# Kernel optimization log

Hardware: AMD Instinct MI355X
Metric: run time of the kernel (lower is better)

Reference implementation:

```python
import jax, jax.numpy as jnp
import numpy as np

N_NODES = 50000
N_EDGES = 800000


def gcn_conv(x, src, dst, W, b, n):
    # PyG GCNConv: add self-loops, symmetric normalization D^-1/2 (A+I) D^-1/2,
    # linear transform, scatter-add aggregation, then bias.
    loop = jnp.arange(n, dtype=src.dtype)
    src2 = jnp.concatenate([src, loop])
    dst2 = jnp.concatenate([dst, loop])
    deg = jax.ops.segment_sum(jnp.ones(src2.shape[0], x.dtype), dst2, num_segments=n)
    dis = jnp.where(deg > 0, jax.lax.rsqrt(jnp.maximum(deg, 1e-12)), 0.0)
    norm = dis[src2] * dis[dst2]                      # [E+N]
    xw = x @ W                                        # [N, out]
    msg = xw[src2] * norm[:, None]                    # [E+N, out] gather
    out = jax.ops.segment_sum(msg, dst2, num_segments=n)  # scatter-add
    return out + b


def setup_inputs() -> dict:
    key = jax.random.key(0)
    ks = jax.random.split(key, 8)
    d_in, d_h, d_out = 128, 128, 10
    x = jax.random.normal(ks[0], (N_NODES, d_in), dtype=jnp.float32)
    edge_index = jax.random.randint(ks[1], (2, N_EDGES), 0, N_NODES, dtype=jnp.int64)
    s = 1.0 / np.sqrt(d_in)
    W1 = jax.random.normal(ks[2], (d_in, d_h), dtype=jnp.float32) * s
    b1 = jnp.zeros((d_h,), jnp.float32)
    W2 = jax.random.normal(ks[3], (d_h, d_h), dtype=jnp.float32) * s
    b2 = jnp.zeros((d_h,), jnp.float32)
    W3 = jax.random.normal(ks[4], (d_h, d_out), dtype=jnp.float32) * s
    b3 = jnp.zeros((d_out,), jnp.float32)
    return {"x": x, "edge_index": edge_index, "W1": W1, "b1": b1,
            "W2": W2, "b2": b2, "W3": W3, "b3": b3}


def reference(x, edge_index, W1, b1, W2, b2, W3, b3):
    n = x.shape[0]
    src, dst = edge_index[0], edge_index[1]
    h = gcn_conv(x, src, dst, W1, b1, n)
    h = jax.nn.relu(h)
    # dropout(p=0.5) is identity in eval mode (training=False)
    h = gcn_conv(h, src, dst, W2, b2, n)
    h = gcn_conv(h, src, dst, W3, b3, n)
    return jax.nn.log_softmax(h, axis=1)
```

## Files before the change

### kernel.cpp

```cpp
#include <hip/hip_runtime.h>
#include <cstdint>
#include <cstddef>


typedef unsigned int uint;
typedef unsigned short u16;
typedef uint  uint4e  __attribute__((ext_vector_type(4)));
typedef float float4e __attribute__((ext_vector_type(4)));
typedef float float2e __attribute__((ext_vector_type(2)));
typedef uint  uint2e  __attribute__((ext_vector_type(2)));
typedef int   int2e   __attribute__((ext_vector_type(2)));
typedef int   int4e   __attribute__((ext_vector_type(4)));
using bf16x8 = __attribute__((ext_vector_type(8))) short;
using f32x4  = __attribute__((ext_vector_type(4))) float;

__device__ __forceinline__ float bf_lo(uint v) { return __uint_as_float(v << 16); }
__device__ __forceinline__ float bf_hi(uint v) { return __uint_as_float(v & 0xffff0000u); }
__device__ __forceinline__ u16 bf16_1(float a) {
    uint ua = __float_as_uint(a);
    ua = (ua + 0x7fffu + ((ua >> 16) & 1u)) >> 16;
    return (u16)ua;
}
__device__ __forceinline__ uint pack_bf2(float a, float b) {
    return (uint)bf16_1(a) | ((uint)bf16_1(b) << 16);
}

__global__ __launch_bounds__(256) void passA_wt(const int* __restrict__ ei, int E,
        int* __restrict__ cntA, int nbkt, int nca,
        const float* __restrict__ W1, const float* __restrict__ W2,
        const float* __restrict__ W3, const float* __restrict__ b2,
        u16* __restrict__ Wt1, float* __restrict__ W23, float* __restrict__ b23) {
    int tid = threadIdx.x, b = blockIdx.x;
    if (b < nca) {
        __shared__ int h[256];
        h[tid] = 0;
        __syncthreads();
        int ch = (E + nca - 1) / nca;
        int beg = b * ch, end = min(beg + ch, E);
        for (int e = beg + tid; e < end; e += 256)
            atomicAdd(&h[ei[E + e] >> 8], 1);
        __syncthreads();
        if (tid < nbkt) cntA[tid * nca + b] = h[tid];
    } else if (b == nca) {
        for (int i = 0; i < 64; ++i) {
            int idx = tid + i * 256;
            int k = idx >> 7, c = idx & 127;
            Wt1[c * 128 + k] = bf16_1(W1[idx]);
        }
        int c = tid >> 4, j0 = tid & 15;
        float acc = 0.f;
        if (c < 10) {
#pragma unroll
            for (int j = 0; j < 128; j += 16)
                acc += b2[j + j0] * W3[(j + j0) * 10 + c];
        }
#pragma unroll
        for (int m = 1; m < 16; m <<= 1) acc += __shfl_xor(acc, m);
        if (c < 10 && j0 == 0) b23[c] = acc;
    } else {
        __shared__ float w3s[1280];
        for (int i = tid; i < 1280; i += 256) w3s[i] = W3[i];
        __syncthreads();
        int idx = (b - nca - 1) * 256 + tid;
        int k = idx / 10, c = idx % 10;
        const float* w2r = W2 + (size_t)k * 128;
        float a0 = 0.f, a1 = 0.f, a2 = 0.f, a3 = 0.f;
#pragma unroll
        for (int j = 0; j < 128; j += 4) {
            a0 += w2r[j + 0] * w3s[(j + 0) * 10 + c];
            a1 += w2r[j + 1] * w3s[(j + 1) * 10 + c];
            a2 += w2r[j + 2] * w3s[(j + 2) * 10 + c];
            a3 += w2r[j + 3] * w3s[(j + 3) * 10 + c];
        }
        W23[idx] = (a0 + a1) + (a2 + a3);
    }
}

__global__ __launch_bounds__(256) void scan1(int* __restrict__ cntA, int nca,
        int* __restrict__ btot) {
    __shared__ int s[256];
    int b = blockIdx.x, tid = threadIdx.x;
    int v = cntA[b * nca + tid];
    s[tid] = v;
    __syncthreads();
    for (int d = 1; d < 256; d <<= 1) {
        int t = (tid >= d) ? s[tid - d] : 0;
        __syncthreads();
        s[tid] += t;
        __syncthreads();
    }
    cntA[b * nca + tid] = s[tid] - v;
    if (tid == 255) btot[b] = s[255];
}

__global__ __launch_bounds__(256) void passB(const int* __restrict__ ei, int E,
        const int* __restrict__ cntA, int nca, int nbkt,
        const int* __restrict__ btot, int2e* __restrict__ ebkt) {
    __shared__ int sc[256];
    __shared__ int cur[256];
    int tid = threadIdx.x, b = blockIdx.x;
    int v = (tid < nbkt) ? btot[tid] : 0;
    sc[tid] = v;
    __syncthreads();
    for (int d = 1; d < 256; d <<= 1) {
        int t = (tid >= d) ? sc[tid - d] : 0;
        __syncthreads();
        sc[tid] += t;
        __syncthreads();
    }
    cur[tid] = (sc[tid] - v) + ((tid < nbkt) ? cntA[tid * nca + b] : 0);
    __syncthreads();
    int ch = (E + nca - 1) / nca;
    int beg = b * ch, end = min(beg + ch, E);
    for (int e = beg + tid; e < end; e += 256) {
        int s = ei[e], d = ei[E + e];
        int pos = atomicAdd(&cur[d >> 8], 1);
        int2e pkt;
        pkt.x = s;
        pkt.y = d;
        ebkt[pos] = pkt;
    }
}

__global__ __launch_bounds__(256) void passC(const int2e* __restrict__ ebkt,
        const int* __restrict__ btot, int2e* __restrict__ esort,
        int* __restrict__ row_ptr, float* __restrict__ dis, int n, int nbkt, int E) {
    __shared__ int sc[256];
    __shared__ int fc[256];
    __shared__ int s_base;
    int k = blockIdx.x, tid = threadIdx.x;
    int bt = (tid < nbkt) ? btot[tid] : 0;
    sc[tid] = bt;
    __syncthreads();
    for (int d = 1; d < 256; d <<= 1) {
        int t = (tid >= d) ? sc[tid - d] : 0;
        __syncthreads();
        sc[tid] += t;
        __syncthreads();
    }
    if (tid == k) s_base = sc[tid] - bt;
    fc[tid] = 0;
    __syncthreads();
    int base = s_base;
    int endb = base + btot[k];
    int node0 = k << 8;
    for (int i = base + tid; i < endb; i += 256)
        atomicAdd(&fc[ebkt[i].y & 255], 1);
    __syncthreads();
    int v = fc[tid];
    sc[tid] = v;
    __syncthreads();
    for (int d = 1; d < 256; d <<= 1) {
        int t = (tid >= d) ? sc[tid - d] : 0;
        __syncthreads();
        sc[tid] += t;
        __syncthreads();
    }
    int excl = sc[tid] - v;
    if (node0 + tid < n) {
        dis[node0 + tid] = rsqrtf((float)(v + 1));
        row_ptr[node0 + tid] = base + excl;
    }
    __syncthreads();
    fc[tid] = base + excl;
    __syncthreads();
    for (int i = base + tid; i < endb; i += 256) {
        int2e ed = ebkt[i];
        int pos = atomicAdd(&fc[ed.y & 255], 1);
        esort[pos] = ed;
    }
    if (k == 0 && tid == 0) row_ptr[n] = E;
}

__global__ __launch_bounds__(256) void gemm_mfma(const float* __restrict__ A,
        const u16* __restrict__ Wt, u16* __restrict__ out, int n) {
    constexpr int LDA = 136;
    __shared__ u16 as[64 * LDA];
    int tid = threadIdx.x;
    int wave = tid >> 6, lane = tid & 63;
    int row0 = blockIdx.x * 64;
    int l16 = lane & 15;
    int krow = (lane >> 4) * 8;

#pragma unroll
    for (int i = 0; i < 8; ++i) {
        int idx = tid + i * 256;
        int r = idx >> 5;
        int q = (idx & 31) * 4;
        float4e v = {0.f, 0.f, 0.f, 0.f};
        if (row0 + r < n)
            v = *reinterpret_cast<const float4e*>(A + (size_t)(row0 + r) * 128 + q);
        uint2e p;
        p.x = pack_bf2(v.x, v.y);
        p.y = pack_bf2(v.z, v.w);
        *reinterpret_cast<uint2e*>(&as[r * LDA + q]) = p;
    }

    bf16x8 b[2][4];
#pragma unroll
    for (int n2 = 0; n2 < 2; ++n2)
#pragma unroll
        for (int kb = 0; kb < 4; ++kb)
            b[n2][kb] = *reinterpret_cast<const bf16x8*>(
                Wt + (size_t)(wave * 32 + n2 * 16 + l16) * 128 + kb * 32 + krow);

    __syncthreads();

    f32x4 acc[4][2] = {};
#pragma unroll
    for (int m = 0; m < 4; ++m) {
#pragma unroll
        for (int kb = 0; kb < 4; ++kb) {
            bf16x8 a = *reinterpret_cast<const bf16x8*>(
                &as[(m * 16 + l16) * LDA + kb * 32 + krow]);
#pragma unroll
            for (int n2 = 0; n2 < 2; ++n2)
                acc[m][n2] = __builtin_amdgcn_mfma_f32_16x16x32_bf16(a, b[n2][kb], acc[m][n2], 0, 0, 0);
        }
    }

    __syncthreads();
    u16* cs = as;
#pragma unroll
    for (int m = 0; m < 4; ++m) {
        int rb = m * 16 + (lane >> 4) * 4;
#pragma unroll
        for (int n2 = 0; n2 < 2; ++n2) {
            int col = wave * 32 + n2 * 16 + l16;
#pragma unroll
            for (int r = 0; r < 4; ++r)
                cs[(rb + r) * 128 + col] = bf16_1(acc[m][n2][r]);
        }
    }
    __syncthreads();
#pragma unroll
    for (int i = 0; i < 4; ++i) {
        int idx = tid + i * 256;
        int r = idx >> 4;
        int q = (idx & 15) * 8;
        if (row0 + r < n)
            *reinterpret_cast<uint4e*>(out + (size_t)(row0 + r) * 128 + q) =
                *reinterpret_cast<const uint4e*>(&cs[r * 128 + q]);
    }
}

__device__ __forceinline__ void gather_accum(const uint* __restrict__ xw,
        const int2e* __restrict__ esort, const float* __restrict__ dis,
        int v, int lane, int beg, int end, float& ax, float& ay) {
    float dv = dis[v];
    int e = beg;
    for (; e + 7 < end; e += 8) {
        int2e ed[8];
        uint vv[8];
        float wd[8];
#pragma unroll
        for (int j = 0; j < 8; ++j) ed[j] = esort[e + j];
#pragma unroll
        for (int j = 0; j < 8; ++j) {
            vv[j] = xw[(size_t)ed[j].x * 64 + lane];
            wd[j] = dis[ed[j].x];
        }
#pragma unroll
        for (int j = 0; j < 8; ++j) {
            float w = wd[j] * dv;
            ax += w * bf_lo(vv[j]);
            ay += w * bf_hi(vv[j]);
        }
    }
    for (; e + 1 < end; e += 2) {
        int2e e0 = esort[e];
        int2e e1 = esort[e + 1];
        uint v0 = xw[(size_t)e0.x * 64 + lane];
        uint v1 = xw[(size_t)e1.x * 64 + lane];
        float w0 = dis[e0.x] * dv, w1 = dis[e1.x] * dv;
        ax += w0 * bf_lo(v0); ay += w0 * bf_hi(v0);
        ax += w1 * bf_lo(v1); ay += w1 * bf_hi(v1);
    }
    if (e < end) {
        int2e e0 = esort[e];
        uint v0 = xw[(size_t)e0.x * 64 + lane];
        float w0 = dis[e0.x] * dv;
        ax += w0 * bf_lo(v0); ay += w0 * bf_hi(v0);
    }
    float wv = dv * dv;
    uint vs = xw[(size_t)v * 64 + lane];
    ax += wv * bf_lo(vs); ay += wv * bf_hi(vs);
}

__global__ __launch_bounds__(256) void agg_proj_kernel(const uint* __restrict__ xw,
        const int* __restrict__ row_ptr, const int2e* __restrict__ esort,
        const float* __restrict__ dis, const float* __restrict__ b1,
        const float* __restrict__ W23, uint* __restrict__ z, int n) {
    int v = (int)((blockIdx.x * blockDim.x + threadIdx.x) >> 6);
    int lane = threadIdx.x & 63;
    if (v >= n) return;
    float ax = 0.f, ay = 0.f;
    gather_accum(xw, esort, dis, v, lane, row_ptr[v], row_ptr[v + 1], ax, ay);
    ax = fmaxf(ax + b1[lane * 2], 0.f);
    ay = fmaxf(ay + b1[lane * 2 + 1], 0.f);
    const float* w0 = W23 + (size_t)lane * 20;
    float p[10];
#pragma unroll
    for (int c = 0; c < 10; ++c) p[c] = ax * w0[c] + ay * w0[10 + c];
#pragma unroll
    for (int c = 0; c < 10; ++c) {
#pragma unroll
        for (int d = 1; d < 64; d <<= 1) p[c] += __shfl_xor(p[c], d);
    }
    if (lane < 5) z[(size_t)v * 5 + lane] = pack_bf2(p[2 * lane], p[2 * lane + 1]);
}

template <int FINAL>
__global__ __launch_bounds__(256) void agg10_kernel(const uint* __restrict__ zin,
        const int* __restrict__ row_ptr, const int2e* __restrict__ esort,
        const float* __restrict__ dis, const float* __restrict__ b23,
        const float* __restrict__ b3, void* __restrict__ zout, int n) {
    int wid = (int)((blockIdx.x * blockDim.x + threadIdx.x) >> 6);
    int lane = threadIdx.x & 63;
    int grp = lane >> 4, gl = lane & 15;
    int v = wid * 4 + grp;
    bool act = (v < n);
    bool dl = (gl < 5);
    int beg = act ? row_ptr[v] : 0;
    int end = act ? row_ptr[v + 1] : 0;
    float dv = act ? dis[v] : 0.f;
    float ax = 0.f, ay = 0.f, sw = 0.f;
    int e = beg;
    for (; e + 7 < end; e += 8) {
        int2e ed[8];
        uint zz[8];
        float wd[8];
#pragma unroll
        for (int j = 0; j < 8; ++j) ed[j] = esort[e + j];
#pragma unroll
        for (int j = 0; j < 8; ++j) {
            zz[j] = dl ? zin[(size_t)ed[j].x * 5 + gl] : 0u;
            wd[j] = dis[ed[j].x];
        }
#pragma unroll
        for (int j = 0; j < 8; ++j) {
            float w = wd[j] * dv;
            ax += w * bf_lo(zz[j]);
            ay += w * bf_hi(zz[j]);
            sw += w;
        }
    }
    for (; e < end; ++e) {
        int2e e0 = esort[e];
        uint z0 = dl ? zin[(size_t)e0.x * 5 + gl] : 0u;
        float w0 = dis[e0.x] * dv;
        ax += w0 * bf_lo(z0);
        ay += w0 * bf_hi(z0);
        sw += w0;
    }
    if (act) {
        float wv = dv * dv;
        uint zs = dl ? zin[(size_t)v * 5 + gl] : 0u;
        ax += wv * bf_lo(zs);
        ay += wv * bf_hi(zs);
        sw += wv;
    }
    if (FINAL == 0) {
        if (act && dl) ((uint*)zout)[(size_t)v * 5 + gl] = pack_bf2(ax, ay);
    } else {
        float pa = 0.f, pb = 0.f;
        if (dl) {
            pa = ax + sw * b23[2 * gl] + b3[2 * gl];
            pb = ay + sw * b23[2 * gl + 1] + b3[2 * gl + 1];
        }
        float m = dl ? fmaxf(pa, pb) : -3.4e38f;
#pragma unroll
        for (int mask = 1; mask < 16; mask <<= 1) m = fmaxf(m, __shfl_xor(m, mask));
        float s = dl ? (__expf(pa - m) + __expf(pb - m)) : 0.f;
#pragma unroll
        for (int mask = 1; mask < 16; mask <<= 1) s += __shfl_xor(s, mask);
        float ls = __logf(s);
        if (act && dl) {
            float2e o = {pa - m - ls, pb - m - ls};
            *reinterpret_cast<float2e*>((float*)zout + (size_t)v * 10 + 2 * gl) = o;
        }
    }
}

extern "C" void kernel_launch(void* const* d_in, const int* in_sizes, int n_in,
                              void* d_out, int out_size, void* d_ws, size_t ws_size,
                              hipStream_t stream) {
    const float* x  = (const float*)d_in[0];
    const int*   ei = (const int*)d_in[1];
    const float* W1 = (const float*)d_in[2];
    const float* b1 = (const float*)d_in[3];
    const float* W2 = (const float*)d_in[4];
    const float* b2 = (const float*)d_in[5];
    const float* W3 = (const float*)d_in[6];
    const float* b3 = (const float*)d_in[7];
    int N = in_sizes[0] / 128;
    int E = in_sizes[1] / 2;
    int NBKT = (N + 255) >> 8;
    const int NCA = 256;

    char* ws = (char*)d_ws;
    size_t off = 0;
    auto alloc = [&](size_t bytes) -> char* {
        char* p = ws + off;
        off = (off + bytes + 255) & ~(size_t)255;
        return p;
    };
    int*   cntA    = (int*)alloc((size_t)NBKT * NCA * 4);
    int*   btot    = (int*)alloc(256 * 4);
    int*   row_ptr = (int*)alloc(((size_t)N + 1) * 4);
    float* dis     = (float*)alloc((size_t)N * 4);
    u16*   Wt1     = (u16*)alloc(128 * 128 * 2);
    float* W23     = (float*)alloc(128 * 10 * 4);
    float* b23     = (float*)alloc(10 * 4);
    int2e* ebkt    = (int2e*)alloc((size_t)E * 8);
    int2e* esort   = (int2e*)alloc((size_t)E * 8);
    uint*  bufA    = (uint*)alloc((size_t)N * 64 * 4);
    uint*  z       = (uint*)alloc((size_t)N * 5 * 4);
    uint*  z2      = (uint*)alloc((size_t)N * 5 * 4);

    passA_wt<<<NCA + 6, 256, 0, stream>>>(ei, E, cntA, NBKT, NCA, W1, W2, W3, b2,
                                          Wt1, W23, b23);
    gemm_mfma<<<(N + 63) / 64, 256, 0, stream>>>(x, Wt1, (u16*)bufA, N);
    scan1<<<NBKT, 256, 0, stream>>>(cntA, NCA, btot);
    passB<<<NCA, 256, 0, stream>>>(ei, E, cntA, NCA, NBKT, btot, ebkt);
    passC<<<NBKT, 256, 0, stream>>>(ebkt, btot, esort, row_ptr, dis, N, NBKT, E);
    agg_proj_kernel<<<(N + 3) / 4, 256, 0, stream>>>(bufA, row_ptr, esort, dis, b1, W23, z, N);
    agg10_kernel<0><<<(N + 15) / 16, 256, 0, stream>>>(z, row_ptr, esort, dis, nullptr, nullptr, z2, N);
    agg10_kernel<1><<<(N + 15) / 16, 256, 0, stream>>>(z2, row_ptr, esort, dis, b23, b3, d_out, N);
}
```

Measured before the change: 129.5 us.

## Slice feature table into 8 column blocks and split aggregation from projection

The GEMM output is stored as eight column slices of 16 bf16 features each, so each slice table is small enough to stay cache-resident. The first aggregation runs one wave per (node, slice), with 8 lanes per edge covering 8 edges in parallel, then reduces across edge groups with shuffles. The fused projection to 10 outputs moves into a separate per-node kernel that holds the weights in shared memory. This trades one extra hidden-feature buffer write and read plus an extra launch for better gather locality and fewer cross-lane reductions.

```diff
diff --git a/kernel.cpp b/kernel.cpp
--- a/kernel.cpp
+++ b/kernel.cpp
@@ -173,7 +173,7 @@
 }
 
 __global__ __launch_bounds__(256) void gemm_mfma(const float* __restrict__ A,
-        const u16* __restrict__ Wt, u16* __restrict__ out, int n) {
+        const u16* __restrict__ Wt, uint* __restrict__ out, int n) {
     constexpr int LDA = 136;
     __shared__ u16 as[64 * LDA];
     int tid = threadIdx.x;
@@ -237,77 +237,84 @@
     for (int i = 0; i < 4; ++i) {
         int idx = tid + i * 256;
         int r = idx >> 4;
-        int q = (idx & 15) * 8;
+        int o = idx & 15;
+        int s = o >> 1;
+        int h = o & 1;
         if (row0 + r < n)
-            *reinterpret_cast<uint4e*>(out + (size_t)(row0 + r) * 128 + q) =
-                *reinterpret_cast<const uint4e*>(&cs[r * 128 + q]);
-    }
-}
-
-__device__ __forceinline__ void gather_accum(const uint* __restrict__ xw,
-        const int2e* __restrict__ esort, const float* __restrict__ dis,
-        int v, int lane, int beg, int end, float& ax, float& ay) {
+            *reinterpret_cast<uint4e*>(out + (size_t)s * n * 8 + (size_t)(row0 + r) * 8 + h * 4) =
+                *reinterpret_cast<const uint4e*>(&cs[r * 128 + o * 8]);
+    }
+}
+
+__global__ __launch_bounds__(256) void agg_slice_kernel(const uint* __restrict__ bufA,
+        const int* __restrict__ row_ptr, const int2e* __restrict__ esort,
+        const float* __restrict__ dis, const float* __restrict__ b1,
+        uint* __restrict__ hout, int n) {
+    int s = blockIdx.x & 7;
+    int v = (int)((blockIdx.x >> 3) * 4 + (threadIdx.x >> 6));
+    int lane = threadIdx.x & 63;
+    if (v >= n) return;
+    int eg = lane >> 3;
+    int dp = lane & 7;
+    const uint* tbl = bufA + (size_t)s * n * 8;
     float dv = dis[v];
+    float ax = 0.f, ay = 0.f;
+    int beg = row_ptr[v], end = row_ptr[v + 1];
     int e = beg;
     for (; e + 7 < end; e += 8) {
-        int2e ed[8];
-        uint vv[8];
-        float wd[8];
-#pragma unroll
-        for (int j = 0; j < 8; ++j) ed[j] = esort[e + j];
-#pragma unroll
-        for (int j = 0; j < 8; ++j) {
-            vv[j] = xw[(size_t)ed[j].x * 64 + lane];
-            wd[j] = dis[ed[j].x];
-        }
-#pragma unroll
-        for (int j = 0; j < 8; ++j) {
-            float w = wd[j] * dv;
-            ax += w * bf_lo(vv[j]);
-            ay += w * bf_hi(vv[j]);
-        }
-    }
-    for (; e + 1 < end; e += 2) {
-        int2e e0 = esort[e];
-        int2e e1 = esort[e + 1];
-        uint v0 = xw[(size_t)e0.x * 64 + lane];
-        uint v1 = xw[(size_t)e1.x * 64 + lane];
-        float w0 = dis[e0.x] * dv, w1 = dis[e1.x] * dv;
-        ax += w0 * bf_lo(v0); ay += w0 * bf_hi(v0);
-        ax += w1 * bf_lo(v1); ay += w1 * bf_hi(v1);
+        int2e ed = esort[e + eg];
+        uint t = tbl[(size_t)ed.x * 8 + dp];
+        float w = dis[ed.x] * dv;
+        ax += w * bf_lo(t);
+        ay += w * bf_hi(t);
     }
     if (e < end) {
-        int2e e0 = esort[e];
-        uint v0 = xw[(size_t)e0.x * 64 + lane];
-        float w0 = dis[e0.x] * dv;
-        ax += w0 * bf_lo(v0); ay += w0 * bf_hi(v0);
-    }
+        int rem = end - e;
+        int2e ed = esort[e + (eg < rem ? eg : 0)];
+        uint t = tbl[(size_t)ed.x * 8 + dp];
+        float w = (eg < rem) ? dis[ed.x] * dv : 0.f;
+        ax += w * bf_lo(t);
+        ay += w * bf_hi(t);
+    }
+    ax += __shfl_xor(ax, 8);  ay += __shfl_xor(ay, 8);
+    ax += __shfl_xor(ax, 16); ay += __shfl_xor(ay, 16);
+    ax += __shfl_xor(ax, 32); ay += __shfl_xor(ay, 32);
+    uint tv = tbl[(size_t)v * 8 + dp];
     float wv = dv * dv;
-    uint vs = xw[(size_t)v * 64 + lane];
-    ax += wv * bf_lo(vs); ay += wv * bf_hi(vs);
-}
-
-__global__ __launch_bounds__(256) void agg_proj_kernel(const uint* __restrict__ xw,
-        const int* __restrict__ row_ptr, const int2e* __restrict__ esort,
-        const float* __restrict__ dis, const float* __restrict__ b1,
+    ax += wv * bf_lo(tv);
+    ay += wv * bf_hi(tv);
+    int d0 = s * 16 + 2 * dp;
+    ax = fmaxf(ax + b1[d0], 0.f);
+    ay = fmaxf(ay + b1[d0 + 1], 0.f);
+    if (eg == 0) hout[(size_t)s * n * 8 + (size_t)v * 8 + dp] = pack_bf2(ax, ay);
+}
+
+__global__ __launch_bounds__(256) void proj_kernel(const uint* __restrict__ hout,
         const float* __restrict__ W23, uint* __restrict__ z, int n) {
-    int v = (int)((blockIdx.x * blockDim.x + threadIdx.x) >> 6);
-    int lane = threadIdx.x & 63;
+    __shared__ float w3s[1280];
+    int tid = threadIdx.x;
+    for (int i = tid; i < 1280; i += 256) w3s[i] = W23[i];
+    __syncthreads();
+    int v = blockIdx.x * 256 + tid;
     if (v >= n) return;
-    float ax = 0.f, ay = 0.f;
-    gather_accum(xw, esort, dis, v, lane, row_ptr[v], row_ptr[v + 1], ax, ay);
-    ax = fmaxf(ax + b1[lane * 2], 0.f);
-    ay = fmaxf(ay + b1[lane * 2 + 1], 0.f);
-    const float* w0 = W23 + (size_t)lane * 20;
-    float p[10];
-#pragma unroll
-    for (int c = 0; c < 10; ++c) p[c] = ax * w0[c] + ay * w0[10 + c];
-#pragma unroll
-    for (int c = 0; c < 10; ++c) {
-#pragma unroll
-        for (int d = 1; d < 64; d <<= 1) p[c] += __shfl_xor(p[c], d);
-    }
-    if (lane < 5) z[(size_t)v * 5 + lane] = pack_bf2(p[2 * lane], p[2 * lane + 1]);
+    float p[10] = {};
+#pragma unroll
+    for (int s = 0; s < 8; ++s) {
+        uint4e c0 = *reinterpret_cast<const uint4e*>(hout + (size_t)s * n * 8 + (size_t)v * 8);
+        uint4e c1 = *reinterpret_cast<const uint4e*>(hout + (size_t)s * n * 8 + (size_t)v * 8 + 4);
+        uint u[8] = {c0.x, c0.y, c0.z, c0.w, c1.x, c1.y, c1.z, c1.w};
+#pragma unroll
+        for (int k = 0; k < 8; ++k) {
+            int d = s * 16 + 2 * k;
+            float lo = bf_lo(u[k]), hi = bf_hi(u[k]);
+#pragma unroll
+            for (int c = 0; c < 10; ++c)
+                p[c] += lo * w3s[d * 10 + c] + hi * w3s[(d + 1) * 10 + c];
+        }
+    }
+#pragma unroll
+    for (int i = 0; i < 5; ++i)
+        z[(size_t)v * 5 + i] = pack_bf2(p[2 * i], p[2 * i + 1]);
 }
 
 template <int FINAL>
@@ -415,16 +422,19 @@
     int2e* ebkt    = (int2e*)alloc((size_t)E * 8);
     int2e* esort   = (int2e*)alloc((size_t)E * 8);
     uint*  bufA    = (uint*)alloc((size_t)N * 64 * 4);
+    uint*  hbuf    = (uint*)alloc((size_t)N * 64 * 4);
     uint*  z       = (uint*)alloc((size_t)N * 5 * 4);
     uint*  z2      = (uint*)alloc((size_t)N * 5 * 4);
 
     passA_wt<<<NCA + 6, 256, 0, stream>>>(ei, E, cntA, NBKT, NCA, W1, W2, W3, b2,
                                           Wt1, W23, b23);
-    gemm_mfma<<<(N + 63) / 64, 256, 0, stream>>>(x, Wt1, (u16*)bufA, N);
+    gemm_mfma<<<(N + 63) / 64, 256, 0, stream>>>(x, Wt1, bufA, N);
     scan1<<<NBKT, 256, 0, stream>>>(cntA, NCA, btot);
     passB<<<NCA, 256, 0, stream>>>(ei, E, cntA, NCA, NBKT, btot, ebkt);
     passC<<<NBKT, 256, 0, stream>>>(ebkt, btot, esort, row_ptr, dis, N, NBKT, E);
-    agg_proj_kernel<<<(N + 3) / 4, 256, 0, stream>>>(bufA, row_ptr, esort, dis, b1, W23, z, N);
+    agg_slice_kernel<<<8 * ((N + 3) / 4), 256, 0, stream>>>(bufA, row_ptr, esort, dis,
+                                                            b1, hbuf, N);
+    proj_kernel<<<(N + 255) / 256, 256, 0, stream>>>(hbuf, W23, z, N);
     agg10_kernel<0><<<(N + 15) / 16, 256, 0, stream>>>(z, row_ptr, esort, dis, nullptr, nullptr, z2, N);
     agg10_kernel<1><<<(N + 15) / 16, 256, 0, stream>>>(z2, row_ptr, esort, dis, b23, b3, d_out, N);
 }
```

After: 214.5 us. +65.6%, slower.
